# Optimization experiments

Hardware: AMD Instinct MI355X
Metric: run time of the kernel (lower is better)

Reference implementation:

```python
import jax, jax.numpy as jnp
import numpy as np

N_NODES = 50000
N_EDGES = 1000000
IN_F = 128
OUT_F = 128
K = 4
NEG_SLOPE = 0.01  # torch nn.LeakyReLU() default
EPS = 1e-8


def setup_inputs() -> dict:
    key = jax.random.key(0)
    k1, k2, k3, k4, k5, k6 = jax.random.split(key, 6)
    x = jax.random.normal(k1, (N_NODES, IN_F), dtype=jnp.float32)
    e = jax.random.uniform(k2, (N_NODES, K), dtype=jnp.float32)
    stdv = 1.0 / np.sqrt(OUT_F)
    weights = jax.random.uniform(k3, (K, IN_F, OUT_F), minval=-stdv, maxval=stdv, dtype=jnp.float32)
    a = jax.random.normal(k4, (K, 2 * OUT_F, 1), dtype=jnp.float32) * 0.1
    # edge_index with no self-loops (remove_self_loops is then a no-op)
    row = jax.random.randint(k5, (N_EDGES,), 0, N_NODES)
    off = jax.random.randint(k6, (N_EDGES,), 1, N_NODES)
    col = (row + off) % N_NODES
    adj = jnp.stack([row, col]).astype(jnp.int64)
    return {"x": x, "e": e, "weights": weights, "a": a, "adj": adj}


def _canet_gat_forward(x, e, weights, a, adj):
    N = x.shape[0]
    out_f = weights.shape[-1]
    # add self loops (input has none)
    loops = jnp.arange(N, dtype=adj.dtype)
    src = jnp.concatenate([adj[0], loops])  # [Et]
    dst = jnp.concatenate([adj[1], loops])  # [Et]

    # per-head projection: [K, N, O]
    h = jnp.einsum('nd,kdo->kno', x, weights)

    # attention logits: a = [a_src; a_dst], logit_e = leakyrelu(h[src].a_src + h[dst].a_dst)
    a_src = a[:, :out_f, 0]   # [K, O]
    a_dst = a[:, out_f:, 0]   # [K, O]
    s_src = jnp.einsum('kno,ko->kn', h, a_src)  # [K, N]
    s_dst = jnp.einsum('kno,ko->kn', h, a_dst)  # [K, N]
    logits = s_src[:, src] + s_dst[:, dst]      # [K, Et]
    logits = jnp.where(logits >= 0, logits, NEG_SLOPE * logits)
    logits_max = jnp.max(logits, axis=1, keepdims=True)  # global max per head
    edge_e = jnp.exp(logits - logits_max)                # [K, Et]

    outputs = []
    for k in range(h.shape[0]):  # small fixed loop over heads (avoids [K,Et,O] blowup)
        denom = jax.ops.segment_sum(edge_e[k], src, num_segments=N) + EPS   # [N]
        msg = edge_e[k][:, None] * h[k][dst]                                # [Et, O]
        hi_k = jax.ops.segment_sum(msg, src, num_segments=N)                # [N, O]
        outputs.append(hi_k / denom[:, None])
    outputs = jnp.stack(outputs, axis=1)  # [N, K, O]

    out = jnp.sum(e[:, :, None] * outputs, axis=1)  # [N, O]
    return out + x  # residual (in_features == out_features)


def reference(x, e, weights, a, adj):
    return _canet_gat_forward(x, e, weights, a, adj)
```

## Files before the change

kernel.cpp:

```cpp
#include <hip/hip_runtime.h>
#include <hip/hip_bf16.h>
#include <cstddef>

#define NN 50000
#define NE 1000000
#define F  128
#define KH 4
#define NEG 0.01f
#define EPSF 1e-8f
#define CAP 64
#define NBE ((NE + 1023) / 1024)
#define NBW 256
#define NBP 256

typedef short bf16x8 __attribute__((ext_vector_type(8)));
typedef float f32x4 __attribute__((ext_vector_type(4)));

__device__ inline ushort f2bf(float f) {
    __hip_bfloat16 b = __float2bfloat16(f);
    return *reinterpret_cast<ushort*>(&b);
}
__device__ inline float2 bf2_to_f2(unsigned int v) {
    union { unsigned int u; float f; } a, b;
    a.u = (v & 0xffffu) << 16;
    b.u = v & 0xffff0000u;
    return make_float2(a.f, b.f);
}
__device__ inline unsigned int packbf(float xl, float xh) {
    return (unsigned int)f2bf(xl) | ((unsigned int)f2bf(xh) << 16);
}
__device__ inline float lk(float v) { return (v >= 0.f) ? v : NEG * v; }

__global__ __launch_bounds__(256) void mega_kernel(const int* __restrict__ adj,
                                                   int* __restrict__ cnt,
                                                   int* __restrict__ bucket,
                                                   const float* __restrict__ W,
                                                   const float* __restrict__ a,
                                                   ushort* __restrict__ wt,
                                                   const float* __restrict__ x,
                                                   unsigned int* __restrict__ xb2,
                                                   float* __restrict__ ssrc4,
                                                   float* __restrict__ sdst4,
                                                   int* __restrict__ mxsi) {
    int b = blockIdx.x;
    if (b < NBE) {
        int base = b * 1024 + threadIdx.x;
        int s[4], d[4], p[4];
        bool v[4];
#pragma unroll
        for (int u = 0; u < 4; u++) {
            int e = base + u * 256;
            v[u] = e < NE;
            int ee = v[u] ? e : 0;
            s[u] = adj[ee];
            d[u] = adj[NE + ee];
        }
#pragma unroll
        for (int u = 0; u < 4; u++) {
            if (v[u]) p[u] = atomicAdd(&cnt[s[u]], 1);
        }
#pragma unroll
        for (int u = 0; u < 4; u++) {
            if (v[u] && p[u] < CAP) bucket[(size_t)s[u] * CAP + p[u]] = d[u];
        }
    } else if (b < NBE + NBW) {
        int i = (b - NBE) * 256 + threadIdx.x;
        int k = i >> 14;
        int dd = (i >> 7) & 127;
        int o = i & 127;
        wt[((size_t)k * F + o) * F + dd] = f2bf(W[i]);
    } else {
        __shared__ float vv_s[8][F];
        for (int j = threadIdx.x; j < 8 * F; j += 256) {
            int side = j >> 9;
            int k = (j >> 7) & 3;
            int dd = j & 127;
            const float4* Wr = (const float4*)(W + (size_t)k * F * F + (size_t)dd * F);
            const float4* ar = (const float4*)(a + (size_t)k * 2 * F + side * F);
            float acc = 0.f;
#pragma unroll 8
            for (int o = 0; o < F / 4; o++) {
                float4 wv = Wr[o], av = ar[o];
                acc += wv.x * av.x + wv.y * av.y + wv.z * av.z + wv.w * av.w;
            }
            vv_s[(size_t)side * 4 + k][dd] = acc;
        }
        __syncthreads();

        int wv = threadIdx.x >> 6, lane = threadIdx.x & 63;
        int gw = (b - NBE - NBW) * 4 + wv;
        const float2* x2 = (const float2*)x;
        float2 vs[4], vd[4];
#pragma unroll
        for (int k = 0; k < 4; k++) {
            vs[k] = *(const float2*)&vv_s[k][2 * lane];
            vd[k] = *(const float2*)&vv_s[4 + k][2 * lane];
        }
        float mx[8];
#pragma unroll
        for (int j = 0; j < 8; j++) mx[j] = 0.f;

        for (int n = gw; n < NN; n += 1024) {
            float2 xv = x2[(size_t)n * 64 + lane];
            xb2[(size_t)n * 64 + lane] = packbf(xv.x, xv.y);
            float s[8];
#pragma unroll
            for (int k = 0; k < 4; k++) {
                s[k]     = xv.x * vs[k].x + xv.y * vs[k].y;
                s[4 + k] = xv.x * vd[k].x + xv.y * vd[k].y;
            }
#pragma unroll
            for (int st = 1; st < 64; st <<= 1) {
#pragma unroll
                for (int j = 0; j < 8; j++) s[j] += __shfl_xor(s[j], st);
            }
            if (lane == 0) {
                *(float4*)&ssrc4[(size_t)n * 4] = make_float4(s[0], s[1], s[2], s[3]);
                *(float4*)&sdst4[(size_t)n * 4] = make_float4(s[4], s[5], s[6], s[7]);
#pragma unroll
                for (int j = 0; j < 8; j++) mx[j] = fmaxf(mx[j], s[j]);
            }
        }
        __shared__ float bmax[4][8];
        if (lane == 0) {
#pragma unroll
            for (int j = 0; j < 8; j++) bmax[wv][j] = mx[j];
        }
        __syncthreads();
        if (threadIdx.x < 8) {
            int j = threadIdx.x;
            float m = fmaxf(fmaxf(bmax[0][j], bmax[1][j]), fmaxf(bmax[2][j], bmax[3][j]));
            atomicMax(&mxsi[j], __float_as_int(m));
        }
    }
}

__global__ __launch_bounds__(256) void aggregate_kernel(const unsigned int* __restrict__ xb2,
                                                        const float* __restrict__ ssrc4,
                                                        const float* __restrict__ sdst4,
                                                        const float* __restrict__ mxs,
                                                        const int* __restrict__ cnt,
                                                        const int* __restrict__ bucket,
                                                        const float* __restrict__ ew,
                                                        unsigned int* __restrict__ z2) {
    int wv = threadIdx.x >> 6, lane = threadIdx.x & 63;
    int n = blockIdx.x * 4 + wv;
    if (n >= NN) return;

    __shared__ int dsh[4][64];
    __shared__ __align__(16) float wsh[4][64][4];

    float4 mxa = *(const float4*)&mxs[0];
    float4 mxb = *(const float4*)&mxs[4];
    float m0 = lk(mxa.x + mxb.x), m1 = lk(mxa.y + mxb.y);
    float m2 = lk(mxa.z + mxb.z), m3 = lk(mxa.w + mxb.w);
    float4 ss  = *(const float4*)&ssrc4[(size_t)n * 4];
    float4 sdn = *(const float4*)&sdst4[(size_t)n * 4];
    float w0s = __expf(lk(ss.x + sdn.x) - m0);
    float w1s = __expf(lk(ss.y + sdn.y) - m1);
    float w2s = __expf(lk(ss.z + sdn.z) - m2);
    float w3s = __expf(lk(ss.w + sdn.w) - m3);

    int deg = min(cnt[n], CAP);
    if (lane < deg) {
        int d = bucket[(size_t)n * CAP + lane];
        dsh[wv][lane] = d;
        float4 sd = *(const float4*)&sdst4[(size_t)d * 4];
        float4 w;
        w.x = __expf(lk(ss.x + sd.x) - m0);
        w.y = __expf(lk(ss.y + sd.y) - m1);
        w.z = __expf(lk(ss.z + sd.z) - m2);
        w.w = __expf(lk(ss.w + sd.w) - m3);
        *(float4*)&wsh[wv][lane][0] = w;
    }

    float a0[4], a1[4], den[4];
    {
        float2 f = bf2_to_f2(xb2[(size_t)n * 64 + lane]);
        a0[0] = w0s * f.x; a1[0] = w0s * f.y; den[0] = w0s;
        a0[1] = w1s * f.x; a1[1] = w1s * f.y; den[1] = w1s;
        a0[2] = w2s * f.x; a1[2] = w2s * f.y; den[2] = w2s;
        a0[3] = w3s * f.x; a1[3] = w3s * f.y; den[3] = w3s;
    }

    for (int i = 0; i < deg; i += 8) {
        int du[8]; float4 wu[8]; unsigned int vu[8];
#pragma unroll
        for (int u = 0; u < 8; u++) {
            int iu = i + u;
            bool val = iu < deg;
            int sel = val ? iu : 0;
            du[u] = dsh[wv][sel];
            float4 w = *(const float4*)&wsh[wv][sel][0];
            wu[u] = val ? w : make_float4(0.f, 0.f, 0.f, 0.f);
        }
#pragma unroll
        for (int u = 0; u < 8; u++) vu[u] = xb2[(size_t)du[u] * 64 + lane];
#pragma unroll
        for (int u = 0; u < 8; u++) {
            float2 f = bf2_to_f2(vu[u]);
            float4 w = wu[u];
            a0[0] += w.x * f.x; a1[0] += w.x * f.y; den[0] += w.x;
            a0[1] += w.y * f.x; a1[1] += w.y * f.y; den[1] += w.y;
            a0[2] += w.z * f.x; a1[2] += w.z * f.y; den[2] += w.z;
            a0[3] += w.w * f.x; a1[3] += w.w * f.y; den[3] += w.w;
        }
    }

    float4 e4 = *(const float4*)&ew[(size_t)n * 4];
    float i0 = e4.x / (den[0] + EPSF);
    float i1 = e4.y / (den[1] + EPSF);
    float i2 = e4.z / (den[2] + EPSF);
    float i3 = e4.w / (den[3] + EPSF);
    size_t zb = (size_t)n * 256;
    z2[zb +   0 + lane] = packbf(a0[0] * i0, a1[0] * i0);
    z2[zb +  64 + lane] = packbf(a0[1] * i1, a1[1] * i1);
    z2[zb + 128 + lane] = packbf(a0[2] * i2, a1[2] * i2);
    z2[zb + 192 + lane] = packbf(a0[3] * i3, a1[3] * i3);
}

#define MT 64
__global__ __launch_bounds__(256) void gemm2_kernel(const ushort* __restrict__ z,
                                                    const ushort* __restrict__ wt,
                                                    const float* __restrict__ x,
                                                    float* __restrict__ out) {
    int row0 = blockIdx.x * MT;
    int tid = threadIdx.x;
    int wave = tid >> 6, lane = tid & 63;
    int quad = lane >> 4, l16 = lane & 15;
    __shared__ ushort ws[F][136];

    int arow = row0 + wave * 16 + l16;
    if (arow >= NN) arow = NN - 1;

    f32x4 acc[8];
#pragma unroll
    for (int i = 0; i < 8; i++) acc[i] = (f32x4){0.f, 0.f, 0.f, 0.f};

    for (int k = 0; k < KH; k++) {
        __syncthreads();
        const ushort* wk = wt + (size_t)k * F * F;
        for (int i = tid; i < F * 16; i += 256) {
            int r = i >> 4, c = (i & 15) * 8;
            *(uint4*)&ws[r][c] = *(const uint4*)&wk[r * F + c];
        }
        __syncthreads();
#pragma unroll
        for (int kt = 0; kt < 4; kt++) {
            int kb = kt * 32 + quad * 8;
            bf16x8 af = *(const bf16x8*)&z[(size_t)arow * 512 + k * F + kb];
#pragma unroll
            for (int ni = 0; ni < 8; ni++) {
                bf16x8 bf = *(const bf16x8*)&ws[ni * 16 + l16][kb];
                acc[ni] = __builtin_amdgcn_mfma_f32_16x16x32_bf16(af, bf, acc[ni], 0, 0, 0);
            }
        }
    }
#pragma unroll
    for (int r = 0; r < 4; r++) {
        int n = row0 + wave * 16 + quad * 4 + r;
        if (n < NN) {
#pragma unroll
            for (int ni = 0; ni < 8; ni++) {
                int o = ni * 16 + l16;
                out[(size_t)n * F + o] = x[(size_t)n * F + o] + acc[ni][r];
            }
        }
    }
}

extern "C" void kernel_launch(void* const* d_in, const int* in_sizes, int n_in,
                              void* d_out, int out_size, void* d_ws, size_t ws_size,
                              hipStream_t stream) {
    const float* x = (const float*)d_in[0];
    const float* e = (const float*)d_in[1];
    const float* W = (const float*)d_in[2];
    const float* a = (const float*)d_in[3];
    const int*   adj = (const int*)d_in[4];
    float* out = (float*)d_out;

    char* ws = (char*)d_ws;
    auto take = [&](size_t bytes) {
        char* p = ws;
        ws += (bytes + 255) & ~(size_t)255;
        return p;
    };
    ushort* z      = (ushort*)take((size_t)NN * KH * F * sizeof(ushort));
    unsigned int* xb2 = (unsigned int*)take((size_t)NN * F * sizeof(ushort));
    ushort* wt     = (ushort*)take((size_t)KH * F * F * sizeof(ushort));
    float* ssrc4   = (float*)take((size_t)NN * 4 * sizeof(float));
    float* sdst4   = (float*)take((size_t)NN * 4 * sizeof(float));
    int*   cnt     = (int*)take((size_t)NN * sizeof(int) + 32);
    float* mxs     = (float*)(cnt + NN);
    int*   bucket  = (int*)take((size_t)NN * CAP * sizeof(int));

    hipMemsetAsync(cnt, 0, (size_t)NN * sizeof(int) + 32, stream);
    mega_kernel<<<NBE + NBW + NBP, 256, 0, stream>>>(adj, cnt, bucket, W, a, wt,
                                                     x, xb2, ssrc4, sdst4, (int*)mxs);
    aggregate_kernel<<<(NN + 3) / 4, 256, 0, stream>>>(xb2, ssrc4, sdst4, mxs, cnt,
                                                       bucket, e, (unsigned int*)z);
    gemm2_kernel<<<(NN + MT - 1) / MT, 256, 0, stream>>>(z, wt, x, out);
}
```

Measured before the change: 270.5 us.

## Split node-score prep into separate kernel with transposed shuffle reduction

After: 289.2 us, median of 2. 6.9% more time.

```diff
diff --git a/kernel.cpp b/kernel.cpp
--- a/kernel.cpp
+++ b/kernel.cpp
@@ -11,7 +11,7 @@
 #define CAP 64
 #define NBE ((NE + 1023) / 1024)
 #define NBW 256
-#define NBP 256
+#define NBP 1024
 
 typedef short bf16x8 __attribute__((ext_vector_type(8)));
 typedef float f32x4 __attribute__((ext_vector_type(4)));
@@ -31,17 +31,13 @@
 }
 __device__ inline float lk(float v) { return (v >= 0.f) ? v : NEG * v; }
 
-__global__ __launch_bounds__(256) void mega_kernel(const int* __restrict__ adj,
-                                                   int* __restrict__ cnt,
-                                                   int* __restrict__ bucket,
-                                                   const float* __restrict__ W,
-                                                   const float* __restrict__ a,
-                                                   ushort* __restrict__ wt,
-                                                   const float* __restrict__ x,
-                                                   unsigned int* __restrict__ xb2,
-                                                   float* __restrict__ ssrc4,
-                                                   float* __restrict__ sdst4,
-                                                   int* __restrict__ mxsi) {
+__global__ __launch_bounds__(256) void bucket_kernel(const int* __restrict__ adj,
+                                                     int* __restrict__ cnt,
+                                                     int* __restrict__ bucket,
+                                                     const float* __restrict__ W,
+                                                     const float* __restrict__ a,
+                                                     ushort* __restrict__ wt,
+                                                     float* __restrict__ vvg) {
     int b = blockIdx.x;
     if (b < NBE) {
         int base = b * 1024 + threadIdx.x;
@@ -70,8 +66,10 @@
         int o = i & 127;
         wt[((size_t)k * F + o) * F + dd] = f2bf(W[i]);
     } else {
-        __shared__ float vv_s[8][F];
-        for (int j = threadIdx.x; j < 8 * F; j += 256) {
+        int j0 = threadIdx.x * 4;
+#pragma unroll
+        for (int ii = 0; ii < 4; ii++) {
+            int j = j0 + ii;
             int side = j >> 9;
             int k = (j >> 7) & 3;
             int dd = j & 127;
@@ -83,56 +81,69 @@
                 float4 wv = Wr[o], av = ar[o];
                 acc += wv.x * av.x + wv.y * av.y + wv.z * av.z + wv.w * av.w;
             }
-            vv_s[(size_t)side * 4 + k][dd] = acc;
-        }
-        __syncthreads();
-
-        int wv = threadIdx.x >> 6, lane = threadIdx.x & 63;
-        int gw = (b - NBE - NBW) * 4 + wv;
-        const float2* x2 = (const float2*)x;
-        float2 vs[4], vd[4];
+            vvg[j] = acc;
+        }
+    }
+}
+
+__global__ __launch_bounds__(256) void prep_kernel(const float* __restrict__ vvg,
+                                                   const float* __restrict__ x,
+                                                   unsigned int* __restrict__ xb2,
+                                                   float* __restrict__ ssrc4,
+                                                   float* __restrict__ sdst4,
+                                                   int* __restrict__ mxsi) {
+    __shared__ float vv_s[8][F];
+    ((float4*)vv_s)[threadIdx.x] = ((const float4*)vvg)[threadIdx.x];
+    __syncthreads();
+
+    int wv = threadIdx.x >> 6, lane = threadIdx.x & 63;
+    int gw = blockIdx.x * 4 + wv;
+    const float2* x2 = (const float2*)x;
+    float2 vs[4], vd[4];
+#pragma unroll
+    for (int k = 0; k < 4; k++) {
+        vs[k] = *(const float2*)&vv_s[k][2 * lane];
+        vd[k] = *(const float2*)&vv_s[4 + k][2 * lane];
+    }
+    int l1 = lane & 1, l2 = lane & 2, l4 = lane & 4;
+    int j = 4 * l1 + l2 + (l4 >> 2);
+    float* sp = (j < 4) ? (ssrc4 + j) : (sdst4 + (j - 4));
+    float mxv = 0.f;
+
+    for (int n = gw; n < NN; n += NBP * 4) {
+        float2 xv = x2[(size_t)n * 64 + lane];
+        xb2[(size_t)n * 64 + lane] = packbf(xv.x, xv.y);
+        float s[8];
 #pragma unroll
         for (int k = 0; k < 4; k++) {
-            vs[k] = *(const float2*)&vv_s[k][2 * lane];
-            vd[k] = *(const float2*)&vv_s[4 + k][2 * lane];
-        }
-        float mx[8];
-#pragma unroll
-        for (int j = 0; j < 8; j++) mx[j] = 0.f;
-
-        for (int n = gw; n < NN; n += 1024) {
-            float2 xv = x2[(size_t)n * 64 + lane];
-            xb2[(size_t)n * 64 + lane] = packbf(xv.x, xv.y);
-            float s[8];
-#pragma unroll
-            for (int k = 0; k < 4; k++) {
-                s[k]     = xv.x * vs[k].x + xv.y * vs[k].y;
-                s[4 + k] = xv.x * vd[k].x + xv.y * vd[k].y;
-            }
-#pragma unroll
-            for (int st = 1; st < 64; st <<= 1) {
-#pragma unroll
-                for (int j = 0; j < 8; j++) s[j] += __shfl_xor(s[j], st);
-            }
-            if (lane == 0) {
-                *(float4*)&ssrc4[(size_t)n * 4] = make_float4(s[0], s[1], s[2], s[3]);
-                *(float4*)&sdst4[(size_t)n * 4] = make_float4(s[4], s[5], s[6], s[7]);
-#pragma unroll
-                for (int j = 0; j < 8; j++) mx[j] = fmaxf(mx[j], s[j]);
-            }
-        }
-        __shared__ float bmax[4][8];
-        if (lane == 0) {
-#pragma unroll
-            for (int j = 0; j < 8; j++) bmax[wv][j] = mx[j];
-        }
-        __syncthreads();
-        if (threadIdx.x < 8) {
-            int j = threadIdx.x;
-            float m = fmaxf(fmaxf(bmax[0][j], bmax[1][j]), fmaxf(bmax[2][j], bmax[3][j]));
-            atomicMax(&mxsi[j], __float_as_int(m));
-        }
-    }
+            s[k]     = xv.x * vs[k].x + xv.y * vs[k].y;
+            s[4 + k] = xv.x * vd[k].x + xv.y * vd[k].y;
+        }
+        float t[4], u[2], v;
+#pragma unroll
+        for (int i = 0; i < 4; i++) {
+            float mine = l1 ? s[4 + i] : s[i];
+            float oth  = __shfl_xor(l1 ? s[i] : s[4 + i], 1);
+            t[i] = mine + oth;
+        }
+#pragma unroll
+        for (int i = 0; i < 2; i++) {
+            float mine = l2 ? t[2 + i] : t[i];
+            float oth  = __shfl_xor(l2 ? t[i] : t[2 + i], 2);
+            u[i] = mine + oth;
+        }
+        {
+            float mine = l4 ? u[1] : u[0];
+            float oth  = __shfl_xor(l4 ? u[0] : u[1], 4);
+            v = mine + oth;
+        }
+        v += __shfl_xor(v, 8);
+        v += __shfl_xor(v, 16);
+        v += __shfl_xor(v, 32);
+        if (lane < 8) sp[(size_t)n * 4] = v;
+        mxv = fmaxf(mxv, v);
+    }
+    if (lane < 8) atomicMax(&mxsi[j], __float_as_int(mxv));
 }
 
 __global__ __launch_bounds__(256) void aggregate_kernel(const unsigned int* __restrict__ xb2,
@@ -293,10 +304,11 @@
     int*   cnt     = (int*)take((size_t)NN * sizeof(int) + 32);
     float* mxs     = (float*)(cnt + NN);
     int*   bucket  = (int*)take((size_t)NN * CAP * sizeof(int));
+    float* vvg     = (float*)take((size_t)8 * F * sizeof(float));
 
     hipMemsetAsync(cnt, 0, (size_t)NN * sizeof(int) + 32, stream);
-    mega_kernel<<<NBE + NBW + NBP, 256, 0, stream>>>(adj, cnt, bucket, W, a, wt,
-                                                     x, xb2, ssrc4, sdst4, (int*)mxs);
+    bucket_kernel<<<NBE + NBW + 1, 256, 0, stream>>>(adj, cnt, bucket, W, a, wt, vvg);
+    prep_kernel<<<NBP, 256, 0, stream>>>(vvg, x, xb2, ssrc4, sdst4, (int*)mxs);
     aggregate_kernel<<<(NN + 3) / 4, 256, 0, stream>>>(xb2, ssrc4, sdst4, mxs, cnt,
                                                        bucket, e, (unsigned int*)z);
     gemm2_kernel<<<(NN + MT - 1) / MT, 256, 0, stream>>>(z, wt, x, out);
```
